# Kernel optimization log

Hardware: AMD Instinct MI355X
Metric: run time of the kernel (lower is better)

## Reference

```python
import jax, jax.numpy as jnp
import numpy as np

KS = 3
N = KS * KS
PAD = 1


def conv2d(x, w, b, stride=1, pad=0):
    out = jax.lax.conv_general_dilated(x, w, (stride, stride), [(pad, pad), (pad, pad)],
                                       dimension_numbers=('NCHW', 'OIHW', 'NCHW'))
    return out + b[None, :, None, None]


def lrelu(x):
    return jnp.where(x > 0, x, 0.2 * x)


# bicubic x2 upsample: half-pixel centers, cubic a=-0.75, replicate edges (matches torch F.interpolate bicubic)
_W_F75 = np.array([-0.03515625, 0.26171875, 0.87890625, -0.10546875], np.float32)  # frac 0.75 (even out idx)
_W_F25 = _W_F75[::-1].copy()  # frac 0.25 (odd out idx)


def _up2_axis(x, axis):
    n = x.shape[axis]
    j = np.arange(2 * n)
    c = (j + 0.5) / 2.0 - 0.5
    i0 = np.floor(c).astype(np.int32)
    taps = np.clip(i0[:, None] + np.arange(-1, 3)[None, :], 0, n - 1)  # [2n,4]
    w = np.where((j % 2 == 0)[:, None], _W_F75[None, :], _W_F25[None, :]).astype(np.float32)
    xm = jnp.moveaxis(x, axis, -1)
    g = xm[..., jnp.asarray(taps)]  # [..., 2n, 4]
    out = jnp.einsum('...jt,jt->...j', g, jnp.asarray(w))
    return jnp.moveaxis(out, -1, axis)


def bicubic_up2(x):
    return _up2_axis(_up2_axis(x, 2), 3)


def head(x, cw, cb, ra_w, ra_b, rb_w, rb_b):
    # Conv5x5 -> LReLU -> ResBlock -> LReLU
    h = lrelu(conv2d(x, cw, cb, pad=2))
    r = conv2d(lrelu(conv2d(h, ra_w, ra_b, pad=1)), rb_w, rb_b, pad=1) + h
    return lrelu(r)


def aligned_forward(x, query, ref, c1_w, c1_b, r1a_w, r1a_b, r1b_w, r1b_b,
                    p1_w, p1_b, r2a_w, r2a_b, r2b_w, r2b_b, p2_w, p2_b):
    q_up = bicubic_up2(query)
    rf = head(ref, c1_w, c1_b, r1a_w, r1a_b, r1b_w, r1b_b)
    qf = head(q_up, c1_w, c1_b, r1a_w, r1a_b, r1b_w, r1b_b)
    cat = jnp.concatenate([rf, qf], axis=1)
    h1 = lrelu(conv2d(cat, p1_w, p1_b, pad=2))
    h1 = lrelu(conv2d(lrelu(conv2d(h1, r2a_w, r2a_b, pad=1)), r2b_w, r2b_b, pad=1) + h1)
    aff = conv2d(h1, p2_w, p2_b, pad=0) + 1.0
    aff = jnp.clip(aff, -3.0, 3.0)
    b, _, h, w = aff.shape
    aff = jnp.transpose(aff, (0, 2, 3, 1))  # [b,h,w,3]
    s_x = aff[..., 0:1]
    s_y = aff[..., 1:2]
    theta = (aff[..., 2:3] - 1.0) * 1.0472
    vals = jnp.array([-1.5, -0.5, 0.5], aff.dtype)  # kernel offsets for ks=3
    pn_x = jnp.repeat(vals, KS)  # [N]
    pn_y = jnp.tile(vals, KS)
    px0 = pn_x * s_x  # [b,h,w,N] scaled kernel offsets
    py0 = pn_y * s_y
    ct = jnp.cos(theta)
    st = jnp.sin(theta)
    rx = px0 * ct - py0 * st  # rotate
    ry = px0 * st + py0 * ct
    px = rx + 1.5 + (jnp.arange(h, dtype=aff.dtype) + 1.0)[None, :, None, None]
    py = ry + 1.5 + (jnp.arange(w, dtype=aff.dtype) + 1.0)[None, None, :, None]
    xp = jnp.pad(x, ((0, 0), (0, 0), (PAD, PAD), (PAD, PAD)), mode='reflect')
    bsz, c, Hp, Wp = xp.shape
    fx = jnp.floor(px)
    fy = jnp.floor(py)
    qltx = jnp.clip(fx, 0, Hp - 1)
    qlty = jnp.clip(fy, 0, Wp - 1)
    qrbx = jnp.clip(fx + 1, 0, Hp - 1)
    qrby = jnp.clip(fy + 1, 0, Wp - 1)
    pxc = jnp.clip(px, 0, Hp - 1)
    pyc = jnp.clip(py, 0, Wp - 1)
    g_lt = (1 + (qltx - pxc)) * (1 + (qlty - pyc))
    g_rb = (1 - (qrbx - pxc)) * (1 - (qrby - pyc))
    g_lb = (1 + (qltx - pxc)) * (1 - (qrby - pyc))
    g_rt = (1 - (qrbx - pxc)) * (1 + (qlty - pyc))
    x_flat = xp.reshape(bsz, c, Hp * Wp)

    def gather(qx, qy):
        idx = (qx.astype(jnp.int32) * Wp + qy.astype(jnp.int32)).reshape(bsz, 1, -1)
        v = jnp.take_along_axis(x_flat, jnp.broadcast_to(idx, (bsz, c, idx.shape[-1])), axis=2)
        return v.reshape(bsz, c, h, w, N)

    align = (g_lt[:, None] * gather(qltx, qlty) + g_rb[:, None] * gather(qrbx, qrby)
             + g_lb[:, None] * gather(qltx, qrby) + g_rt[:, None] * gather(qrbx, qlty))
    # [b,c,h,w,N] -> [b,c,h*ks,w*ks]
    out = align.reshape(bsz, c, h, w, KS, KS).transpose(0, 1, 2, 4, 3, 5).reshape(bsz, c, h * KS, w * KS)
    return out


def setup_inputs() -> dict:
    key = jax.random.key(0)
    ks = jax.random.split(key, 10)

    def W(k, shape):
        fan_in = int(np.prod(shape[1:]))
        return jax.random.normal(k, shape, jnp.float32) / np.sqrt(fan_in)

    return {
        'x': jax.random.normal(ks[0], (2, 32, 256, 256), jnp.float32),
        'query': jax.random.normal(ks[1], (2, 3, 128, 128), jnp.float32),
        'ref': jax.random.normal(ks[2], (2, 3, 256, 256), jnp.float32),
        'c1_w': W(ks[3], (32, 3, 5, 5)), 'c1_b': jnp.zeros((32,), jnp.float32),
        'r1a_w': W(ks[4], (32, 32, 3, 3)), 'r1a_b': jnp.zeros((32,), jnp.float32),
        'r1b_w': W(ks[5], (32, 32, 3, 3)), 'r1b_b': jnp.zeros((32,), jnp.float32),
        'p1_w': W(ks[6], (32, 64, 5, 5)), 'p1_b': jnp.zeros((32,), jnp.float32),
        'r2a_w': W(ks[7], (32, 32, 3, 3)), 'r2a_b': jnp.zeros((32,), jnp.float32),
        'r2b_w': W(ks[8], (32, 32, 3, 3)), 'r2b_b': jnp.zeros((32,), jnp.float32),
        'p2_w': W(ks[9], (3, 32, 1, 1)), 'p2_b': jnp.zeros((3,), jnp.float32),
    }


def reference(x, query, ref, c1_w, c1_b, r1a_w, r1a_b, r1b_w, r1b_b,
              p1_w, p1_b, r2a_w, r2a_b, r2b_w, r2b_b, p2_w, p2_b):
    return aligned_forward(x, query, ref, c1_w, c1_b, r1a_w, r1a_b, r1b_w, r1b_b,
                           p1_w, p1_b, r2a_w, r2a_b, r2b_w, r2b_b, p2_w, p2_b)
```

## Files before the change

kernel.cpp:

```cpp
#include <hip/hip_runtime.h>
#include <math.h>

#define HW 65536

__device__ __forceinline__ float lrelu_f(float v) { return v > 0.f ? v : 0.2f * v; }

__global__ __launch_bounds__(256) void repack_all(
    const float* __restrict__ c1_w, float* __restrict__ wr_c1,
    const float* __restrict__ r1a_w, float* __restrict__ wr_r1a,
    const float* __restrict__ r1b_w, float* __restrict__ wr_r1b,
    const float* __restrict__ p1_w, float* __restrict__ wr_p1,
    const float* __restrict__ r2a_w, float* __restrict__ wr_r2a,
    const float* __restrict__ r2b_w, float* __restrict__ wr_r2b) {
  int i = blockIdx.x * 256 + threadIdx.x;
  const float* src;
  float* dst;
  int IC, KK, base;
  if (i < 2400)        { src = c1_w;  dst = wr_c1;  IC = 3;  KK = 25; base = 0; }
  else if (i < 11616)  { src = r1a_w; dst = wr_r1a; IC = 32; KK = 9;  base = 2400; }
  else if (i < 20832)  { src = r1b_w; dst = wr_r1b; IC = 32; KK = 9;  base = 11616; }
  else if (i < 72032)  { src = p1_w;  dst = wr_p1;  IC = 64; KK = 25; base = 20832; }
  else if (i < 81248)  { src = r2a_w; dst = wr_r2a; IC = 32; KK = 9;  base = 72032; }
  else if (i < 90464)  { src = r2b_w; dst = wr_r2b; IC = 32; KK = 9;  base = 81248; }
  else return;
  int j = i - base;
  int ickk = IC * KK;
  int o = j / ickk;
  int r = j - o * ickk;
  int ic = r / KK;
  int k = r - ic * KK;
  dst[((ic * 4 + (o >> 3)) * KK + k) * 8 + (o & 7)] = src[j];
}

__global__ __launch_bounds__(256) void up2_kernel(const float* __restrict__ q,
                                                  float* __restrict__ out) {
  int gid = blockIdx.x * blockDim.x + threadIdx.x;
  if (gid >= 2 * 3 * HW) return;
  int x = gid & 255;
  int y = (gid >> 8) & 255;
  int pc = gid >> 16;
  const float F[4] = {-0.03515625f, 0.26171875f, 0.87890625f, -0.10546875f};
  int iy[4], ix[4];
  float wy[4], wx[4];
  {
    int k = y >> 1; bool even = !(y & 1); int i0 = even ? k - 1 : k;
#pragma unroll
    for (int t = 0; t < 4; ++t) {
      int ii = i0 - 1 + t;
      iy[t] = min(max(ii, 0), 127);
      wy[t] = even ? F[t] : F[3 - t];
    }
  }
  {
    int k = x >> 1; bool even = !(x & 1); int i0 = even ? k - 1 : k;
#pragma unroll
    for (int t = 0; t < 4; ++t) {
      int ii = i0 - 1 + t;
      ix[t] = min(max(ii, 0), 127);
      wx[t] = even ? F[t] : F[3 - t];
    }
  }
  const float* qp = q + pc * 16384;
  float s = 0.f;
#pragma unroll
  for (int i = 0; i < 4; ++i) {
    float rs = 0.f;
#pragma unroll
    for (int j = 0; j < 4; ++j) rs = fmaf(wx[j], qp[iy[i] * 128 + ix[j]], rs);
    s = fmaf(wy[i], rs, s);
  }
  out[gid] = s;
}


__global__ __launch_bounds__(256) void conv5_c1(const float* __restrict__ in,
                                                const float* __restrict__ wr,
                                                const float* __restrict__ bias,
                                                float* __restrict__ out) {
  __shared__ float sm[3][12][36];
  int blk = blockIdx.x;
  int b = blk >> 10;
  int ocg = (blk >> 8) & 3;
  int tile = blk & 255;
  int ty0 = (tile >> 3) * 8, tx0 = (tile & 7) * 32;
  int tid = threadIdx.x;
  for (int i = tid; i < 3 * 432; i += 256) {
    int ic = i / 432;
    int rem = i - ic * 432;
    int r = rem / 36;
    int c = rem - r * 36;
    int gy = ty0 + r - 2, gx = tx0 + c - 2;
    float v = 0.f;
    if ((unsigned)gy < 256u && (unsigned)gx < 256u) v = in[(b * 3 + ic) * HW + gy * 256 + gx];
    sm[ic][r][c] = v;
  }
  __syncthreads();
  int lane = tid & 63;
  int wv = __builtin_amdgcn_readfirstlane(tid >> 6);
  int py = 2 * wv + (lane >> 5), px = lane & 31;
  float acc[8];
#pragma unroll
  for (int o = 0; o < 8; ++o) acc[o] = bias[ocg * 8 + o];
#pragma unroll
  for (int ic = 0; ic < 3; ++ic) {
    const float* wp = wr + (ic * 4 + ocg) * 200;
#pragma unroll
    for (int ky = 0; ky < 5; ++ky)
#pragma unroll
      for (int kx = 0; kx < 5; ++kx) {
        float v = sm[ic][py + ky][px + kx];
        const float* w8 = wp + (ky * 5 + kx) * 8;
#pragma unroll
        for (int o = 0; o < 8; ++o) acc[o] = fmaf(v, w8[o], acc[o]);
      }
  }
  int y = ty0 + py, x = tx0 + px;
#pragma unroll
  for (int o = 0; o < 8; ++o)
    out[(b * 32 + ocg * 8 + o) * HW + y * 256 + x] = lrelu_f(acc[o]);
}

template <bool RES>
__global__ __launch_bounds__(256) void conv3_32(const float* __restrict__ in, int in_cs,
                                                const float* __restrict__ wr,
                                                const float* __restrict__ bias,
                                                const float* __restrict__ res,
                                                float* __restrict__ out, int out_cs,
                                                int out_co) {
  __shared__ float sm[8][10][34];
  int blk = blockIdx.x;
  int b = blk >> 10;
  int ocg = (blk >> 8) & 3;
  int tile = blk & 255;
  int ty0 = (tile >> 3) * 8, tx0 = (tile & 7) * 32;
  int tid = threadIdx.x;
  int lane = tid & 63;
  int wv = __builtin_amdgcn_readfirstlane(tid >> 6);
  int py = 2 * wv + (lane >> 5), px = lane & 31;
  float acc[8];
#pragma unroll
  for (int o = 0; o < 8; ++o) acc[o] = bias[ocg * 8 + o];
#pragma unroll 1
  for (int ch = 0; ch < 4; ++ch) {
    __syncthreads();
    for (int i = tid; i < 8 * 340; i += 256) {
      int ic = i / 340;
      int rem = i - ic * 340;
      int r = rem / 34;
      int c = rem - r * 34;
      int gy = ty0 + r - 1, gx = tx0 + c - 1;
      float v = 0.f;
      if ((unsigned)gy < 256u && (unsigned)gx < 256u)
        v = in[(b * in_cs + ch * 8 + ic) * HW + gy * 256 + gx];
      sm[ic][r][c] = v;
    }
    __syncthreads();
#pragma unroll 2
    for (int ic = 0; ic < 8; ++ic) {
      const float* wp = wr + ((ch * 8 + ic) * 4 + ocg) * 72;
#pragma unroll
      for (int ky = 0; ky < 3; ++ky)
#pragma unroll
        for (int kx = 0; kx < 3; ++kx) {
          float v = sm[ic][py + ky][px + kx];
          const float* w8 = wp + (ky * 3 + kx) * 8;
#pragma unroll
          for (int o = 0; o < 8; ++o) acc[o] = fmaf(v, w8[o], acc[o]);
        }
    }
  }
  int y = ty0 + py, x = tx0 + px;
  int co = out_co + ocg * 8;
#pragma unroll
  for (int o = 0; o < 8; ++o) {
    float rv = acc[o];
    if (RES) rv += res[(b * 32 + ocg * 8 + o) * HW + y * 256 + x];
    out[(b * out_cs + co + o) * HW + y * 256 + x] = lrelu_f(rv);
  }
}

__global__ __launch_bounds__(256) void conv5_p1(const float* __restrict__ in,
                                                const float* __restrict__ wr,
                                                const float* __restrict__ bias,
                                                float* __restrict__ out) {
  __shared__ float sm[8][12][36];
  int blk = blockIdx.x;
  int b = blk >> 10;
  int ocg = (blk >> 8) & 3;
  int tile = blk & 255;
  int ty0 = (tile >> 3) * 8, tx0 = (tile & 7) * 32;
  int tid = threadIdx.x;
  int lane = tid & 63;
  int wv = __builtin_amdgcn_readfirstlane(tid >> 6);
  int py = 2 * wv + (lane >> 5), px = lane & 31;
  float acc[8];
#pragma unroll
  for (int o = 0; o < 8; ++o) acc[o] = bias[ocg * 8 + o];
#pragma unroll 1
  for (int ch = 0; ch < 8; ++ch) {
    __syncthreads();
    for (int i = tid; i < 8 * 432; i += 256) {
      int ic = i / 432;
      int rem = i - ic * 432;
      int r = rem / 36;
      int c = rem - r * 36;
      int gy = ty0 + r - 2, gx = tx0 + c - 2;
      float v = 0.f;
      if ((unsigned)gy < 256u && (unsigned)gx < 256u)
        v = in[(b * 64 + ch * 8 + ic) * HW + gy * 256 + gx];
      sm[ic][r][c] = v;
    }
    __syncthreads();
#pragma unroll 2
    for (int ic = 0; ic < 8; ++ic) {
      const float* wp = wr + ((ch * 8 + ic) * 4 + ocg) * 200;
#pragma unroll
      for (int ky = 0; ky < 5; ++ky)
#pragma unroll
        for (int kx = 0; kx < 5; ++kx) {
          float v = sm[ic][py + ky][px + kx];
          const float* w8 = wp + (ky * 5 + kx) * 8;
#pragma unroll
          for (int o = 0; o < 8; ++o) acc[o] = fmaf(v, w8[o], acc[o]);
        }
    }
  }
  int y = ty0 + py, x = tx0 + px;
#pragma unroll
  for (int o = 0; o < 8; ++o)
    out[(b * 32 + ocg * 8 + o) * HW + y * 256 + x] = lrelu_f(acc[o]);
}

__global__ __launch_bounds__(256) void p2_aff(const float* __restrict__ h2,
                                              const float* __restrict__ w,
                                              const float* __restrict__ bias,
                                              float4* __restrict__ par) {
  int gid = blockIdx.x * 256 + threadIdx.x;
  int b = gid >> 16;
  int p = gid & 65535;
  float a0 = bias[0], a1 = bias[1], a2 = bias[2];
  for (int c = 0; c < 32; ++c) {
    float v = h2[(b * 32 + c) * HW + p];
    a0 = fmaf(v, w[c], a0);
    a1 = fmaf(v, w[32 + c], a1);
    a2 = fmaf(v, w[64 + c], a2);
  }
  a0 = fminf(fmaxf(a0 + 1.f, -3.f), 3.f);
  a1 = fminf(fmaxf(a1 + 1.f, -3.f), 3.f);
  a2 = fminf(fmaxf(a2 + 1.f, -3.f), 3.f);
  float th = (a2 - 1.f) * 1.0472f;
  float4 o;
  o.x = a0;
  o.y = a1;
  o.z = cosf(th);
  o.w = sinf(th);
  par[gid] = o;
}

__device__ __forceinline__ int refl_idx(int k) {
  int s = k - 1;
  s = s < 0 ? -s : s;
  s = s > 255 ? 510 - s : s;
  return s;
}

__global__ __launch_bounds__(256) void sample_kernel(const float* __restrict__ x,
                                                     const float4* __restrict__ par,
                                                     float* __restrict__ out) {
  int gid = blockIdx.x * 256 + threadIdx.x;
  int xw = gid & 255;
  int y = (gid >> 8) & 255;
  int cg = (gid >> 16) & 3;
  int b = gid >> 18;
  float4 pr = par[(b << 16) + y * 256 + xw];
  float sx = pr.x, sy = pr.y, ct = pr.z, st = pr.w;
  int off[9][4];
  float g[9][4];
#pragma unroll
  for (int ki = 0; ki < 3; ++ki)
#pragma unroll
    for (int kj = 0; kj < 3; ++kj) {
      int n = ki * 3 + kj;
      float px0 = ((float)ki - 1.5f) * sx;
      float py0 = ((float)kj - 1.5f) * sy;
      float px = px0 * ct - py0 * st + 1.5f + (float)(y + 1);
      float py = px0 * st + py0 * ct + 1.5f + (float)(xw + 1);
      float fx = floorf(px), fy = floorf(py);
      float x0f = fminf(fmaxf(fx, 0.f), 257.f);
      float x1f = fminf(fmaxf(fx + 1.f, 0.f), 257.f);
      float y0f = fminf(fmaxf(fy, 0.f), 257.f);
      float y1f = fminf(fmaxf(fy + 1.f, 0.f), 257.f);
      float pxc = fminf(fmaxf(px, 0.f), 257.f);
      float pyc = fminf(fmaxf(py, 0.f), 257.f);
      float dx0 = 1.f + (x0f - pxc), dx1 = 1.f - (x1f - pxc);
      float dy0 = 1.f + (y0f - pyc), dy1 = 1.f - (y1f - pyc);
      g[n][0] = dx0 * dy0;
      g[n][1] = dx1 * dy1;
      g[n][2] = dx0 * dy1;
      g[n][3] = dx1 * dy0;
      int xi0 = refl_idx((int)x0f), xi1 = refl_idx((int)x1f);
      int yi0 = refl_idx((int)y0f), yi1 = refl_idx((int)y1f);
      off[n][0] = xi0 * 256 + yi0;
      off[n][1] = xi1 * 256 + yi1;
      off[n][2] = xi0 * 256 + yi1;
      off[n][3] = xi1 * 256 + yi0;
    }
#pragma unroll 1
  for (int cc = 0; cc < 8; ++cc) {
    int c = cg * 8 + cc;
    const float* xp = x + (size_t)(b * 32 + c) * HW;
    float* op = out + ((size_t)(b * 32 + c) * 768 + 3 * y) * 768 + 3 * xw;
#pragma unroll
    for (int ki = 0; ki < 3; ++ki) {
#pragma unroll
      for (int kj = 0; kj < 3; ++kj) {
        int n = ki * 3 + kj;
        float v = g[n][0] * xp[off[n][0]] + g[n][1] * xp[off[n][1]] +
                  g[n][2] * xp[off[n][2]] + g[n][3] * xp[off[n][3]];
        op[ki * 768 + kj] = v;
      }
    }
  }
}

extern "C" void kernel_launch(void* const* d_in, const int* in_sizes, int n_in,
                              void* d_out, int out_size, void* d_ws, size_t ws_size,
                              hipStream_t stream) {
  const float* x = (const float*)d_in[0];
  const float* query = (const float*)d_in[1];
  const float* ref = (const float*)d_in[2];
  const float* c1_w = (const float*)d_in[3];
  const float* c1_b = (const float*)d_in[4];
  const float* r1a_w = (const float*)d_in[5];
  const float* r1a_b = (const float*)d_in[6];
  const float* r1b_w = (const float*)d_in[7];
  const float* r1b_b = (const float*)d_in[8];
  const float* p1_w = (const float*)d_in[9];
  const float* p1_b = (const float*)d_in[10];
  const float* r2a_w = (const float*)d_in[11];
  const float* r2a_b = (const float*)d_in[12];
  const float* r2b_w = (const float*)d_in[13];
  const float* r2b_b = (const float*)d_in[14];
  const float* p2_w = (const float*)d_in[15];
  const float* p2_b = (const float*)d_in[16];
  float* out = (float*)d_out;

  float* ws = (float*)d_ws;
  float* qup = ws;
  float* cat = qup + 393216;
  float* t1 = cat + 8388608;
  float* t2 = t1 + 4194304;
  float* h1 = t2 + 4194304;
  float4* par = (float4*)(h1 + 4194304);
  float* wr_c1 = (float*)(par + 131072);
  float* wr_r1a = wr_c1 + 2400;
  float* wr_r1b = wr_r1a + 9216;
  float* wr_p1 = wr_r1b + 9216;
  float* wr_r2a = wr_p1 + 51200;
  float* wr_r2b = wr_r2a + 9216;

  repack_all<<<354, 256, 0, stream>>>(c1_w, wr_c1, r1a_w, wr_r1a, r1b_w, wr_r1b,
                                      p1_w, wr_p1, r2a_w, wr_r2a, r2b_w, wr_r2b);

  up2_kernel<<<1536, 256, 0, stream>>>(query, qup);

  conv5_c1<<<2048, 256, 0, stream>>>(ref, wr_c1, c1_b, t1);
  conv3_32<false><<<2048, 256, 0, stream>>>(t1, 32, wr_r1a, r1a_b, nullptr, t2, 32, 0);
  conv3_32<true><<<2048, 256, 0, stream>>>(t2, 32, wr_r1b, r1b_b, t1, cat, 64, 0);

  conv5_c1<<<2048, 256, 0, stream>>>(qup, wr_c1, c1_b, t1);
  conv3_32<false><<<2048, 256, 0, stream>>>(t1, 32, wr_r1a, r1a_b, nullptr, t2, 32, 0);
  conv3_32<true><<<2048, 256, 0, stream>>>(t2, 32, wr_r1b, r1b_b, t1, cat, 64, 32);

  conv5_p1<<<2048, 256, 0, stream>>>(cat, wr_p1, p1_b, h1);
  conv3_32<false><<<2048, 256, 0, stream>>>(h1, 32, wr_r2a, r2a_b, nullptr, t2, 32, 0);
  conv3_32<true><<<2048, 256, 0, stream>>>(t2, 32, wr_r2b, r2b_b, h1, t1, 32, 0);

  p2_aff<<<512, 256, 0, stream>>>(t1, p2_w, p2_b, par);

  sample_kernel<<<2048, 256, 0, stream>>>(x, par, out);
}
```

Baseline: 884.7 us.

## Register-block conv kernels: 4 pixels × 8 channels per thread, all channels per block

The direct conv kernels now have each thread compute a 1×4 strip of pixels for 8 output channels, with each of the 4 waves owning one output-channel group. A block therefore covers all 32 output channels, so the input tile is staged into shared memory once instead of four times. Shared-memory windows are read as float4 and reused across the kx taps, and outputs are written as float4, which cuts LDS and global traffic per FMA. The costs are a much larger shared tile (51 KB for conv3, 61 KB for conv5_p1), which lowers occupancy, and a quarter as many blocks.

```diff
diff --git a/kernel.cpp b/kernel.cpp
--- a/kernel.cpp
+++ b/kernel.cpp
@@ -77,18 +77,17 @@
                                                 const float* __restrict__ wr,
                                                 const float* __restrict__ bias,
                                                 float* __restrict__ out) {
-  __shared__ float sm[3][12][36];
+  __shared__ float sm[3][12][40];
   int blk = blockIdx.x;
-  int b = blk >> 10;
-  int ocg = (blk >> 8) & 3;
+  int b = blk >> 8;
   int tile = blk & 255;
   int ty0 = (tile >> 3) * 8, tx0 = (tile & 7) * 32;
   int tid = threadIdx.x;
-  for (int i = tid; i < 3 * 432; i += 256) {
-    int ic = i / 432;
-    int rem = i - ic * 432;
-    int r = rem / 36;
-    int c = rem - r * 36;
+  for (int i = tid; i < 3 * 480; i += 256) {
+    int ic = i / 480;
+    int rem = i - ic * 480;
+    int r = rem / 40;
+    int c = rem - r * 40;
     int gy = ty0 + r - 2, gx = tx0 + c - 2;
     float v = 0.f;
     if ((unsigned)gy < 256u && (unsigned)gx < 256u) v = in[(b * 3 + ic) * HW + gy * 256 + gx];
@@ -97,27 +96,41 @@
   __syncthreads();
   int lane = tid & 63;
   int wv = __builtin_amdgcn_readfirstlane(tid >> 6);
-  int py = 2 * wv + (lane >> 5), px = lane & 31;
-  float acc[8];
-#pragma unroll
-  for (int o = 0; o < 8; ++o) acc[o] = bias[ocg * 8 + o];
+  int row = lane >> 3, colg = lane & 7;
+  int px0 = colg * 4;
+  float acc[4][8];
+#pragma unroll
+  for (int j = 0; j < 4; ++j)
+#pragma unroll
+    for (int o = 0; o < 8; ++o) acc[j][o] = bias[wv * 8 + o];
 #pragma unroll
   for (int ic = 0; ic < 3; ++ic) {
-    const float* wp = wr + (ic * 4 + ocg) * 200;
-#pragma unroll
-    for (int ky = 0; ky < 5; ++ky)
+    const float* wp = wr + (ic * 4 + wv) * 200;
+#pragma unroll
+    for (int ky = 0; ky < 5; ++ky) {
+      const float* srow = &sm[ic][row + ky][px0];
+      float4 wa = *(const float4*)srow;
+      float4 wb = *(const float4*)(srow + 4);
+      float win[8] = {wa.x, wa.y, wa.z, wa.w, wb.x, wb.y, wb.z, wb.w};
 #pragma unroll
       for (int kx = 0; kx < 5; ++kx) {
-        float v = sm[ic][py + ky][px + kx];
         const float* w8 = wp + (ky * 5 + kx) * 8;
 #pragma unroll
-        for (int o = 0; o < 8; ++o) acc[o] = fmaf(v, w8[o], acc[o]);
+        for (int o = 0; o < 8; ++o) {
+          float wt = w8[o];
+#pragma unroll
+          for (int j = 0; j < 4; ++j) acc[j][o] = fmaf(win[j + kx], wt, acc[j][o]);
+        }
       }
-  }
-  int y = ty0 + py, x = tx0 + px;
-#pragma unroll
-  for (int o = 0; o < 8; ++o)
-    out[(b * 32 + ocg * 8 + o) * HW + y * 256 + x] = lrelu_f(acc[o]);
+    }
+  }
+  int y = ty0 + row, x = tx0 + px0;
+#pragma unroll
+  for (int o = 0; o < 8; ++o) {
+    float4 r4 = make_float4(lrelu_f(acc[0][o]), lrelu_f(acc[1][o]),
+                            lrelu_f(acc[2][o]), lrelu_f(acc[3][o]));
+    *(float4*)&out[(b * 32 + wv * 8 + o) * HW + y * 256 + x] = r4;
+  }
 }
 
 template <bool RES>
@@ -127,108 +140,131 @@
                                                 const float* __restrict__ res,
                                                 float* __restrict__ out, int out_cs,
                                                 int out_co) {
-  __shared__ float sm[8][10][34];
+  __shared__ float sm[32][10][40];
   int blk = blockIdx.x;
-  int b = blk >> 10;
-  int ocg = (blk >> 8) & 3;
+  int b = blk >> 8;
+  int tile = blk & 255;
+  int ty0 = (tile >> 3) * 8, tx0 = (tile & 7) * 32;
+  int tid = threadIdx.x;
+  for (int i = tid; i < 32 * 400; i += 256) {
+    int ic = i / 400;
+    int rem = i - ic * 400;
+    int r = rem / 40;
+    int c = rem - r * 40;
+    int gy = ty0 + r - 1, gx = tx0 + c - 1;
+    float v = 0.f;
+    if ((unsigned)gy < 256u && (unsigned)gx < 256u)
+      v = in[(b * in_cs + ic) * HW + gy * 256 + gx];
+    sm[ic][r][c] = v;
+  }
+  __syncthreads();
+  int lane = tid & 63;
+  int wv = __builtin_amdgcn_readfirstlane(tid >> 6);
+  int row = lane >> 3, colg = lane & 7;
+  int px0 = colg * 4;
+  float acc[4][8];
+#pragma unroll
+  for (int j = 0; j < 4; ++j)
+#pragma unroll
+    for (int o = 0; o < 8; ++o) acc[j][o] = bias[wv * 8 + o];
+#pragma unroll 4
+  for (int ic = 0; ic < 32; ++ic) {
+    const float* wp = wr + (ic * 4 + wv) * 72;
+#pragma unroll
+    for (int ky = 0; ky < 3; ++ky) {
+      const float* srow = &sm[ic][row + ky][px0];
+      float4 wa = *(const float4*)srow;
+      float4 wb = *(const float4*)(srow + 4);
+      float win[8] = {wa.x, wa.y, wa.z, wa.w, wb.x, wb.y, wb.z, wb.w};
+#pragma unroll
+      for (int kx = 0; kx < 3; ++kx) {
+        const float* w8 = wp + (ky * 3 + kx) * 8;
+#pragma unroll
+        for (int o = 0; o < 8; ++o) {
+          float wt = w8[o];
+#pragma unroll
+          for (int j = 0; j < 4; ++j) acc[j][o] = fmaf(win[j + kx], wt, acc[j][o]);
+        }
+      }
+    }
+  }
+  int y = ty0 + row, x = tx0 + px0;
+  int co = out_co + wv * 8;
+#pragma unroll
+  for (int o = 0; o < 8; ++o) {
+    float4 r4 = make_float4(acc[0][o], acc[1][o], acc[2][o], acc[3][o]);
+    if (RES) {
+      float4 rr = *(const float4*)&res[(b * 32 + wv * 8 + o) * HW + y * 256 + x];
+      r4.x += rr.x; r4.y += rr.y; r4.z += rr.z; r4.w += rr.w;
+    }
+    r4.x = lrelu_f(r4.x); r4.y = lrelu_f(r4.y); r4.z = lrelu_f(r4.z); r4.w = lrelu_f(r4.w);
+    *(float4*)&out[(b * out_cs + co + o) * HW + y * 256 + x] = r4;
+  }
+}
+
+__global__ __launch_bounds__(256) void conv5_p1(const float* __restrict__ in,
+                                                const float* __restrict__ wr,
+                                                const float* __restrict__ bias,
+                                                float* __restrict__ out) {
+  __shared__ float sm[32][12][40];
+  int blk = blockIdx.x;
+  int b = blk >> 8;
   int tile = blk & 255;
   int ty0 = (tile >> 3) * 8, tx0 = (tile & 7) * 32;
   int tid = threadIdx.x;
   int lane = tid & 63;
   int wv = __builtin_amdgcn_readfirstlane(tid >> 6);
-  int py = 2 * wv + (lane >> 5), px = lane & 31;
-  float acc[8];
-#pragma unroll
-  for (int o = 0; o < 8; ++o) acc[o] = bias[ocg * 8 + o];
+  int row = lane >> 3, colg = lane & 7;
+  int px0 = colg * 4;
+  float acc[4][8];
+#pragma unroll
+  for (int j = 0; j < 4; ++j)
+#pragma unroll
+    for (int o = 0; o < 8; ++o) acc[j][o] = bias[wv * 8 + o];
 #pragma unroll 1
-  for (int ch = 0; ch < 4; ++ch) {
+  for (int ch = 0; ch < 2; ++ch) {
     __syncthreads();
-    for (int i = tid; i < 8 * 340; i += 256) {
-      int ic = i / 340;
-      int rem = i - ic * 340;
-      int r = rem / 34;
-      int c = rem - r * 34;
-      int gy = ty0 + r - 1, gx = tx0 + c - 1;
-      float v = 0.f;
-      if ((unsigned)gy < 256u && (unsigned)gx < 256u)
-        v = in[(b * in_cs + ch * 8 + ic) * HW + gy * 256 + gx];
-      sm[ic][r][c] = v;
-    }
-    __syncthreads();
-#pragma unroll 2
-    for (int ic = 0; ic < 8; ++ic) {
-      const float* wp = wr + ((ch * 8 + ic) * 4 + ocg) * 72;
-#pragma unroll
-      for (int ky = 0; ky < 3; ++ky)
-#pragma unroll
-        for (int kx = 0; kx < 3; ++kx) {
-          float v = sm[ic][py + ky][px + kx];
-          const float* w8 = wp + (ky * 3 + kx) * 8;
-#pragma unroll
-          for (int o = 0; o < 8; ++o) acc[o] = fmaf(v, w8[o], acc[o]);
-        }
-    }
-  }
-  int y = ty0 + py, x = tx0 + px;
-  int co = out_co + ocg * 8;
-#pragma unroll
-  for (int o = 0; o < 8; ++o) {
-    float rv = acc[o];
-    if (RES) rv += res[(b * 32 + ocg * 8 + o) * HW + y * 256 + x];
-    out[(b * out_cs + co + o) * HW + y * 256 + x] = lrelu_f(rv);
-  }
-}
-
-__global__ __launch_bounds__(256) void conv5_p1(const float* __restrict__ in,
-                                                const float* __restrict__ wr,
-                                                const float* __restrict__ bias,
-                                                float* __restrict__ out) {
-  __shared__ float sm[8][12][36];
-  int blk = blockIdx.x;
-  int b = blk >> 10;
-  int ocg = (blk >> 8) & 3;
-  int tile = blk & 255;
-  int ty0 = (tile >> 3) * 8, tx0 = (tile & 7) * 32;
-  int tid = threadIdx.x;
-  int lane = tid & 63;
-  int wv = __builtin_amdgcn_readfirstlane(tid >> 6);
-  int py = 2 * wv + (lane >> 5), px = lane & 31;
-  float acc[8];
-#pragma unroll
-  for (int o = 0; o < 8; ++o) acc[o] = bias[ocg * 8 + o];
-#pragma unroll 1
-  for (int ch = 0; ch < 8; ++ch) {
-    __syncthreads();
-    for (int i = tid; i < 8 * 432; i += 256) {
-      int ic = i / 432;
-      int rem = i - ic * 432;
-      int r = rem / 36;
-      int c = rem - r * 36;
+    for (int i = tid; i < 32 * 480; i += 256) {
+      int ic = i / 480;
+      int rem = i - ic * 480;
+      int r = rem / 40;
+      int c = rem - r * 40;
       int gy = ty0 + r - 2, gx = tx0 + c - 2;
       float v = 0.f;
       if ((unsigned)gy < 256u && (unsigned)gx < 256u)
-        v = in[(b * 64 + ch * 8 + ic) * HW + gy * 256 + gx];
+        v = in[(b * 64 + ch * 32 + ic) * HW + gy * 256 + gx];
       sm[ic][r][c] = v;
     }
     __syncthreads();
 #pragma unroll 2
-    for (int ic = 0; ic < 8; ++ic) {
-      const float* wp = wr + ((ch * 8 + ic) * 4 + ocg) * 200;
-#pragma unroll
-      for (int ky = 0; ky < 5; ++ky)
+    for (int ic = 0; ic < 32; ++ic) {
+      const float* wp = wr + ((ch * 32 + ic) * 4 + wv) * 200;
+#pragma unroll
+      for (int ky = 0; ky < 5; ++ky) {
+        const float* srow = &sm[ic][row + ky][px0];
+        float4 wa = *(const float4*)srow;
+        float4 wb = *(const float4*)(srow + 4);
+        float win[8] = {wa.x, wa.y, wa.z, wa.w, wb.x, wb.y, wb.z, wb.w};
 #pragma unroll
         for (int kx = 0; kx < 5; ++kx) {
-          float v = sm[ic][py + ky][px + kx];
           const float* w8 = wp + (ky * 5 + kx) * 8;
 #pragma unroll
-          for (int o = 0; o < 8; ++o) acc[o] = fmaf(v, w8[o], acc[o]);
+          for (int o = 0; o < 8; ++o) {
+            float wt = w8[o];
+#pragma unroll
+            for (int j = 0; j < 4; ++j) acc[j][o] = fmaf(win[j + kx], wt, acc[j][o]);
+          }
         }
-    }
-  }
-  int y = ty0 + py, x = tx0 + px;
-#pragma unroll
-  for (int o = 0; o < 8; ++o)
-    out[(b * 32 + ocg * 8 + o) * HW + y * 256 + x] = lrelu_f(acc[o]);
+      }
+    }
+  }
+  int y = ty0 + row, x = tx0 + px0;
+#pragma unroll
+  for (int o = 0; o < 8; ++o) {
+    float4 r4 = make_float4(lrelu_f(acc[0][o]), lrelu_f(acc[1][o]),
+                            lrelu_f(acc[2][o]), lrelu_f(acc[3][o]));
+    *(float4*)&out[(b * 32 + wv * 8 + o) * HW + y * 256 + x] = r4;
+  }
 }
 
 __global__ __launch_bounds__(256) void p2_aff(const float* __restrict__ h2,
@@ -364,17 +400,17 @@
 
   up2_kernel<<<1536, 256, 0, stream>>>(query, qup);
 
-  conv5_c1<<<2048, 256, 0, stream>>>(ref, wr_c1, c1_b, t1);
-  conv3_32<false><<<2048, 256, 0, stream>>>(t1, 32, wr_r1a, r1a_b, nullptr, t2, 32, 0);
-  conv3_32<true><<<2048, 256, 0, stream>>>(t2, 32, wr_r1b, r1b_b, t1, cat, 64, 0);
-
-  conv5_c1<<<2048, 256, 0, stream>>>(qup, wr_c1, c1_b, t1);
-  conv3_32<false><<<2048, 256, 0, stream>>>(t1, 32, wr_r1a, r1a_b, nullptr, t2, 32, 0);
-  conv3_32<true><<<2048, 256, 0, stream>>>(t2, 32, wr_r1b, r1b_b, t1, cat, 64, 32);
-
-  conv5_p1<<<2048, 256, 0, stream>>>(cat, wr_p1, p1_b, h1);
-  conv3_32<false><<<2048, 256, 0, stream>>>(h1, 32, wr_r2a, r2a_b, nullptr, t2, 32, 0);
-  conv3_32<true><<<2048, 256, 0, stream>>>(t2, 32, wr_r2b, r2b_b, h1, t1, 32, 0);
+  conv5_c1<<<512, 256, 0, stream>>>(ref, wr_c1, c1_b, t1);
+  conv3_32<false><<<512, 256, 0, stream>>>(t1, 32, wr_r1a, r1a_b, nullptr, t2, 32, 0);
+  conv3_32<true><<<512, 256, 0, stream>>>(t2, 32, wr_r1b, r1b_b, t1, cat, 64, 0);
+
+  conv5_c1<<<512, 256, 0, stream>>>(qup, wr_c1, c1_b, t1);
+  conv3_32<false><<<512, 256, 0, stream>>>(t1, 32, wr_r1a, r1a_b, nullptr, t2, 32, 0);
+  conv3_32<true><<<512, 256, 0, stream>>>(t2, 32, wr_r1b, r1b_b, t1, cat, 64, 32);
+
+  conv5_p1<<<512, 256, 0, stream>>>(cat, wr_p1, p1_b, h1);
+  conv3_32<false><<<512, 256, 0, stream>>>(h1, 32, wr_r2a, r2a_b, nullptr, t2, 32, 0);
+  conv3_32<true><<<512, 256, 0, stream>>>(t2, 32, wr_r2b, r2b_b, h1, t1, 32, 0);
 
   p2_aff<<<512, 256, 0, stream>>>(t1, p2_w, p2_b, par);
 
```

New measurement: 844.3 us. 4.6% less time.
